# Optimization experiments

Hardware: AMD Instinct MI355X
Metric: run time of the kernel (lower is better)

## Reference

```python
import jax, jax.numpy as jnp
import numpy as np

S, B, D, H, L = 512, 64, 1024, 1024, 2
EPS = 1e-5  # torch LayerNorm default


def setup_inputs() -> dict:
    key = jax.random.key(0)
    ks = jax.random.split(key, 6)
    gain = (1.0 / H) ** 0.5  # matches LSTM._init uniform(-gain, gain)
    return {
        "inputs": jax.random.normal(ks[0], (S, B, D), jnp.float32),
        "h0": jax.random.normal(ks[1], (L, B, H), jnp.float32),
        "c0": jax.random.normal(ks[2], (L, B, H), jnp.float32),
        "wx": jax.random.uniform(ks[3], (L, D, 4 * H), jnp.float32, -gain, gain),
        "wh": jax.random.uniform(ks[4], (L, H, 4 * H), jnp.float32, -gain, gain),
        "bias": jax.random.uniform(ks[5], (L, 4 * H), jnp.float32, -gain, gain),
        "ln_gamma": jnp.ones((L, 4, H), jnp.float32),
        "ln_beta": jnp.zeros((L, 4, H), jnp.float32),
    }


def _run_layer(x, h, c, wx_l, wh_l, b_l, g_l, bb_l):
    # Precompute the input projection for all timesteps (same math as per-step matmul).
    xg = jnp.einsum('sbd,dk->sbk', x, wx_l) + b_l  # [S, B, 4H]

    def step(carry, xg_t):
        h, c = carry
        gate = xg_t + h @ wh_l                      # [B, 4H]
        gate = gate.reshape(-1, 4, H)               # [B, 4, H] per-gate
        mu = gate.mean(-1, keepdims=True)
        var = gate.var(-1, keepdims=True)           # biased, as torch LayerNorm
        gate = (gate - mu) * jax.lax.rsqrt(var + EPS) * g_l + bb_l
        i, f, o, u = gate[:, 0], gate[:, 1], gate[:, 2], gate[:, 3]
        c = jax.nn.sigmoid(f) * c + jax.nn.sigmoid(i) * jnp.tanh(u)
        h = jax.nn.sigmoid(o) * jnp.tanh(c)
        return (h, c), h

    (h, c), ys = jax.lax.scan(step, (h, c), xg)
    return ys, h, c


def reference(inputs, h0, c0, wx, wh, bias, ln_gamma, ln_beta):
    x = inputs
    hs, cs = [], []
    for l in range(L):  # small fixed layer loop (structurally distinct weights)
        x, h, c = _run_layer(x, h0[l], c0[l], wx[l], wh[l], bias[l],
                             ln_gamma[l], ln_beta[l])
        hs.append(h)
        cs.append(c)
    # matches (x, [stacked h, stacked c]) with list_next_state=False
    return x, jnp.stack(hs, 0), jnp.stack(cs, 0)
```

## Files before the change

kernel.cpp:

```cpp
#include <hip/hip_runtime.h>
#include <cstdint>
#include <cstddef>

#define SEQ 512
#define BAT 64
#define DIM 1024
#define HID 1024
#define NLAYER 2
#define NGATE 4096
#define EPS_LN 1e-5f
#define KSPLIT 12
#define PART_STRIDE (BAT * NGATE)
#define LO_SCALE 4096.0f
#define LO_INV (1.0f / 4096.0f)

typedef __attribute__((ext_vector_type(8))) _Float16 f16x8;
typedef __attribute__((ext_vector_type(4))) float f32x4;

__device__ __forceinline__ unsigned short f2h(float f) {
    _Float16 h = (_Float16)f;
    unsigned short u; __builtin_memcpy(&u, &h, 2); return u;
}
__device__ __forceinline__ float h2f(unsigned short u) {
    _Float16 h; __builtin_memcpy(&h, &u, 2); return (float)h;
}


__global__ void init_hc_kernel(const float* __restrict__ h0,
                               const float* __restrict__ c0,
                               float* __restrict__ hbuf,
                               float* __restrict__ cbuf) {
    int i = blockIdx.x * blockDim.x + threadIdx.x;
    hbuf[i] = h0[i];
    cbuf[i] = c0[i];
}

__global__ __launch_bounds__(256) void prepack_w_kernel(
    const float* __restrict__ wx, const float* __restrict__ wh,
    unsigned short* __restrict__ wp)
{
    int gid = blockIdx.x * 256 + threadIdx.x;
    int lane = gid & 63;
    int kc   = (gid >> 6) & 31;
    int nt   = (gid >> 11) & 255;
    int mat  = (gid >> 19) & 1;
    int l    = (gid >> 20) & 1;
    const float* src = (mat ? wh : wx) + (size_t)l * ((size_t)DIM * NGATE);
    int col = nt * 16 + (lane & 15);
    int kr0 = kc * 32 + 8 * (lane >> 4);
    unsigned hp[4], lp[4];
    #pragma unroll
    for (int i = 0; i < 4; i++) {
        float v0 = src[(size_t)(kr0 + 2 * i) * NGATE + col];
        float v1 = src[(size_t)(kr0 + 2 * i + 1) * NGATE + col];
        unsigned short h0 = f2h(v0), h1 = f2h(v1);
        unsigned short l0 = f2h(LO_SCALE * (v0 - h2f(h0)));
        unsigned short l1 = f2h(LO_SCALE * (v1 - h2f(h1)));
        hp[i] = (unsigned)h0 | ((unsigned)h1 << 16);
        lp[i] = (unsigned)l0 | ((unsigned)l1 << 16);
    }
    size_t inner = (((size_t)nt * 32 + kc) * 64 + lane) * 8;
    unsigned short* dh = wp + (((size_t)(l * 4 + mat * 2 + 0)) << 22) + inner;
    unsigned short* dl = wp + (((size_t)(l * 4 + mat * 2 + 1)) << 22) + inner;
    *(uint4*)dh = make_uint4(hp[0], hp[1], hp[2], hp[3]);
    *(uint4*)dl = make_uint4(lp[0], lp[1], lp[2], lp[3]);
}

template<bool DUAL>
__device__ __forceinline__ void gates_body(
    const float* __restrict__ A0, const float* __restrict__ A1,
    const unsigned short* __restrict__ wpl, float* __restrict__ part,
    unsigned short* a_hi, unsigned short* a_lo)
{
    const int ntb = blockIdx.x;
    const int kb  = blockIdx.y;
    int mat, k0, klen;
    if (DUAL) { mat = kb >> 2;       k0 = (kb & 3) * 256; klen = 256; }
    else      { mat = (kb >> 1) & 1; k0 = (kb & 1) * 512; klen = 512; }
    const float* __restrict__ Asrc = mat ? A1 : A0;
    const unsigned short* __restrict__ Wbase =
        wpl + (((size_t)(mat * 2 + (DUAL ? 0 : 1))) << 22);

    const int tid  = threadIdx.x;
    const int lane = tid & 63;
    const int w    = tid >> 6;
    const int m0w  = (w >> 1) * 32;
    const int nh   = w & 1;
    const int lrow = lane & 15;
    const int lg   = lane >> 4;

    f32x4 acc[2][4];
    f32x4 accl[2][4];
    #pragma unroll
    for (int mi = 0; mi < 2; mi++)
        #pragma unroll
        for (int ni = 0; ni < 4; ni++) {
            acc[mi][ni] = (f32x4){0.f, 0.f, 0.f, 0.f};
            accl[mi][ni] = (f32x4){0.f, 0.f, 0.f, 0.f};
        }

    const int sr = tid >> 2;
    const int sq = (tid & 3) * 32;

    for (int kc0 = 0; kc0 < klen; kc0 += 128) {
        __syncthreads();
        {
            const float* s = Asrc + (size_t)sr * 1024 + k0 + kc0 + sq;
            float4 q[8];
            #pragma unroll
            for (int i = 0; i < 8; i++) q[i] = *(const float4*)(s + 4 * i);
            unsigned hp[16], lp[16];
            #pragma unroll
            for (int i = 0; i < 8; i++) {
                unsigned short h0 = f2h(q[i].x), h1 = f2h(q[i].y);
                unsigned short h2 = f2h(q[i].z), h3 = f2h(q[i].w);
                hp[2 * i]     = (unsigned)h0 | ((unsigned)h1 << 16);
                hp[2 * i + 1] = (unsigned)h2 | ((unsigned)h3 << 16);
                if (DUAL) {
                    unsigned short l0 = f2h(LO_SCALE * (q[i].x - h2f(h0)));
                    unsigned short l1 = f2h(LO_SCALE * (q[i].y - h2f(h1)));
                    unsigned short l2 = f2h(LO_SCALE * (q[i].z - h2f(h2)));
                    unsigned short l3 = f2h(LO_SCALE * (q[i].w - h2f(h3)));
                    lp[2 * i]     = (unsigned)l0 | ((unsigned)l1 << 16);
                    lp[2 * i + 1] = (unsigned)l2 | ((unsigned)l3 << 16);
                }
            }
            unsigned base = sr * 256 + sq * 2;
            #pragma unroll
            for (int i = 0; i < 4; i++) {
                unsigned off = (base + 16 * i) ^ ((sr & 7) << 4);
                *(uint4*)((char*)a_hi + off) =
                    make_uint4(hp[4 * i], hp[4 * i + 1], hp[4 * i + 2], hp[4 * i + 3]);
                if (DUAL)
                    *(uint4*)((char*)a_lo + off) =
                        make_uint4(lp[4 * i], lp[4 * i + 1], lp[4 * i + 2], lp[4 * i + 3]);
            }
        }
        __syncthreads();

        const int kcgb = (k0 + kc0) >> 5;
        #pragma unroll
        for (int kk = 0; kk < 4; kk++) {
            f16x8 bfr[4];
            #pragma unroll
            for (int ni = 0; ni < 4; ni++) {
                int ntg = ntb * 8 + nh * 4 + ni;
                const unsigned short* wptr =
                    Wbase + ((((size_t)ntg * 32) + (size_t)(kcgb + kk)) * 64 + lane) * 8;
                bfr[ni] = *(const f16x8*)wptr;
            }
            f16x8 ah[2], al[2];
            #pragma unroll
            for (int mi = 0; mi < 2; mi++) {
                int row = m0w + mi * 16 + lrow;
                unsigned off = ((unsigned)(row * 256 + kk * 64 + lg * 16)) ^ ((row & 7) << 4);
                ah[mi] = *(const f16x8*)((const char*)a_hi + off);
                if (DUAL) al[mi] = *(const f16x8*)((const char*)a_lo + off);
            }
            #pragma unroll
            for (int mi = 0; mi < 2; mi++)
                #pragma unroll
                for (int ni = 0; ni < 4; ni++) {
                    acc[mi][ni] = __builtin_amdgcn_mfma_f32_16x16x32_f16(
                        ah[mi], bfr[ni], acc[mi][ni], 0, 0, 0);
                    if (DUAL)
                        accl[mi][ni] = __builtin_amdgcn_mfma_f32_16x16x32_f16(
                            al[mi], bfr[ni], accl[mi][ni], 0, 0, 0);
                }
        }
    }

    float* __restrict__ pp = part + (size_t)kb * PART_STRIDE;
    #pragma unroll
    for (int mi = 0; mi < 2; mi++)
        #pragma unroll
        for (int ni = 0; ni < 4; ni++) {
            int brow = m0w + mi * 16 + 4 * lg;
            int col  = ntb * 128 + nh * 64 + ni * 16 + lrow;
            #pragma unroll
            for (int r = 0; r < 4; r++) {
                float v = DUAL ? (acc[mi][ni][r] + accl[mi][ni][r] * LO_INV)
                               : (acc[mi][ni][r] * LO_INV);
                pp[(size_t)(brow + r) * NGATE + col] = v;
            }
        }
}

__global__ __launch_bounds__(256) void gates_mfma_kernel(
    const float* __restrict__ A0,
    const float* __restrict__ A1,
    const unsigned short* __restrict__ wpl,
    float* __restrict__ part)
{
    __shared__ __align__(16) unsigned short a_hi[64 * 128];
    __shared__ __align__(16) unsigned short a_lo[64 * 128];
    if (blockIdx.y < 8) gates_body<true>(A0, A1, wpl, part, a_hi, a_lo);
    else                gates_body<false>(A0, A1, wpl, part, a_hi, a_lo);
}

__global__ __launch_bounds__(1024) void update_kernel(
    const float* __restrict__ part,
    const float* __restrict__ bias,
    const float* __restrict__ gamma,
    const float* __restrict__ beta,
    float* __restrict__ cbuf,
    float* __restrict__ hbuf,
    float* __restrict__ y_out,
    float* __restrict__ hs_out,
    float* __restrict__ cs_out)
{
    int b = blockIdx.x;
    int j = threadIdx.x;
    float raw[4], s[4], q[4];
    #pragma unroll
    for (int g = 0; g < 4; g++) {
        int col = g * 1024 + j;
        float v = bias[col];
        #pragma unroll
        for (int p = 0; p < KSPLIT; p++)
            v += part[(size_t)p * PART_STRIDE + (size_t)b * 4096 + col];
        raw[g] = v; s[g] = v; q[g] = v * v;
    }
    #pragma unroll
    for (int off = 32; off > 0; off >>= 1) {
        #pragma unroll
        for (int g = 0; g < 4; g++) {
            s[g] += __shfl_down(s[g], off);
            q[g] += __shfl_down(q[g], off);
        }
    }
    __shared__ float red[16][8];
    __shared__ float stats[8];
    int wave = j >> 6, lane = j & 63;
    if (lane == 0) {
        #pragma unroll
        for (int g = 0; g < 4; g++) { red[wave][g] = s[g]; red[wave][4 + g] = q[g]; }
    }
    __syncthreads();
    if (j == 0) {
        float ts[8] = {0,0,0,0,0,0,0,0};
        for (int w = 0; w < 16; w++)
            for (int g = 0; g < 8; g++) ts[g] += red[w][g];
        #pragma unroll
        for (int g = 0; g < 4; g++) {
            float mu  = ts[g] * (1.0f / 1024.0f);
            float var = ts[4 + g] * (1.0f / 1024.0f) - mu * mu;
            stats[g] = mu;
            stats[4 + g] = rsqrtf(fmaxf(var, 0.0f) + EPS_LN);
        }
    }
    __syncthreads();
    float gh[4];
    #pragma unroll
    for (int g = 0; g < 4; g++) {
        int col = g * 1024 + j;
        gh[g] = (raw[g] - stats[g]) * stats[4 + g] * gamma[col] + beta[col];
    }
    float c_old = cbuf[b * 1024 + j];
    float ig = 1.f / (1.f + __expf(-gh[0]));
    float fg = 1.f / (1.f + __expf(-gh[1]));
    float og = 1.f / (1.f + __expf(-gh[2]));
    float c_new = fg * c_old + ig * tanhf(gh[3]);
    float h_new = og * tanhf(c_new);
    cbuf[b * 1024 + j] = c_new;
    hbuf[b * 1024 + j] = h_new;
    y_out[b * 1024 + j] = h_new;
    if (hs_out) { hs_out[b * 1024 + j] = h_new; cs_out[b * 1024 + j] = c_new; }
}


extern "C" void kernel_launch(void* const* d_in, const int* in_sizes, int n_in,
                              void* d_out, int out_size, void* d_ws, size_t ws_size,
                              hipStream_t stream) {
    const float* inputs = (const float*)d_in[0];
    const float* h0     = (const float*)d_in[1];
    const float* c0     = (const float*)d_in[2];
    const float* wx     = (const float*)d_in[3];
    const float* wh     = (const float*)d_in[4];
    const float* bias   = (const float*)d_in[5];
    const float* gamma  = (const float*)d_in[6];
    const float* beta   = (const float*)d_in[7];
    float* dout = (float*)d_out;

    unsigned short* wp = (unsigned short*)d_ws;
    float* part = (float*)(wp + ((size_t)8 << 22));
    float* hbuf = part + (size_t)KSPLIT * PART_STRIDE;
    float* cbuf = hbuf + NLAYER * BAT * HID;

    prepack_w_kernel<<<8192, 256, 0, stream>>>(wx, wh, wp);
    init_hc_kernel<<<512, 256, 0, stream>>>(h0, c0, hbuf, cbuf);

    const int BH = BAT * HID;
    const int XOUT = SEQ * BAT * HID;
    for (int t = 0; t < SEQ; t++) {
        for (int l = 0; l < NLAYER; l++) {
            const float* a0 = (l == 0) ? (inputs + (size_t)t * BH)
                                       : (dout + (size_t)t * BH);
            gates_mfma_kernel<<<dim3(32, KSPLIT), 256, 0, stream>>>(
                a0, hbuf + l * BH, wp + ((size_t)l << 24), part);
            update_kernel<<<64, 1024, 0, stream>>>(
                part,
                bias + l * 4096, gamma + l * 4096, beta + l * 4096,
                cbuf + l * BH, hbuf + l * BH,
                dout + (size_t)t * BH,
                (t == SEQ - 1) ? (dout + XOUT + l * BH) : nullptr,
                (t == SEQ - 1) ? (dout + XOUT + NLAYER * BH + l * BH) : nullptr);
        }
    }
}
```

Before: 25.20 ms.

## Stage whole K-slice of activations once, halve N tile, double-buffer weight loads

The gates kernel now converts and stores its entire K slice of activations (256 or 512 columns) to shared memory in a single pass, with one barrier instead of a barrier-separated loop of 128-column chunks. Each block now covers 64 gate columns instead of 128, so the grid doubles to 64x12 blocks, and launch bounds request 2 blocks per CU. Weight fragments are register double-buffered, with the next K group's load issued before the current MFMAs. The aim is more parallelism across the MI355X's CUs and less sync and load latency per step. The cost is each block redoing the activation fp16 conversion for half as many columns, plus a 64 KB shared buffer that may limit occupancy.

```diff
diff --git a/kernel.cpp b/kernel.cpp
--- a/kernel.cpp
+++ b/kernel.cpp
@@ -70,13 +70,15 @@
 __device__ __forceinline__ void gates_body(
     const float* __restrict__ A0, const float* __restrict__ A1,
     const unsigned short* __restrict__ wpl, float* __restrict__ part,
-    unsigned short* a_hi, unsigned short* a_lo)
+    unsigned short* __restrict__ abuf)
 {
+    constexpr int KLEN = DUAL ? 256 : 512;
+    constexpr int G = KLEN / 32;
     const int ntb = blockIdx.x;
     const int kb  = blockIdx.y;
-    int mat, k0, klen;
-    if (DUAL) { mat = kb >> 2;       k0 = (kb & 3) * 256; klen = 256; }
-    else      { mat = (kb >> 1) & 1; k0 = (kb & 1) * 512; klen = 512; }
+    int mat, k0;
+    if (DUAL) { mat = kb >> 2;       k0 = (kb & 3) * 256; }
+    else      { mat = (kb >> 1) & 1; k0 = (kb & 1) * 512; }
     const float* __restrict__ Asrc = mat ? A1 : A0;
     const unsigned short* __restrict__ Wbase =
         wpl + (((size_t)(mat * 2 + (DUAL ? 0 : 1))) << 22);
@@ -89,94 +91,99 @@
     const int lrow = lane & 15;
     const int lg   = lane >> 4;
 
-    f32x4 acc[2][4];
-    f32x4 accl[2][4];
+    unsigned short* __restrict__ alo = abuf + 64 * 256;
+
+    {
+        const int sr = tid >> 2;
+        const int sq = (tid & 3) * (KLEN / 4);
+        const float* s = Asrc + (size_t)sr * 1024 + k0 + sq;
+        const unsigned rowb = (unsigned)sr * (KLEN * 2);
+        const unsigned sw = (unsigned)((sr & 7) << 4);
+        #pragma unroll
+        for (int j = 0; j < KLEN / 32; j++) {
+            float4 a = *(const float4*)(s + 8 * j);
+            float4 b = *(const float4*)(s + 8 * j + 4);
+            unsigned short h[8];
+            h[0] = f2h(a.x); h[1] = f2h(a.y); h[2] = f2h(a.z); h[3] = f2h(a.w);
+            h[4] = f2h(b.x); h[5] = f2h(b.y); h[6] = f2h(b.z); h[7] = f2h(b.w);
+            uint4 hv = make_uint4((unsigned)h[0] | ((unsigned)h[1] << 16),
+                                  (unsigned)h[2] | ((unsigned)h[3] << 16),
+                                  (unsigned)h[4] | ((unsigned)h[5] << 16),
+                                  (unsigned)h[6] | ((unsigned)h[7] << 16));
+            unsigned off = (rowb + (unsigned)(sq + 8 * j) * 2) ^ sw;
+            *(uint4*)((char*)abuf + off) = hv;
+            if (DUAL) {
+                unsigned short l[8];
+                l[0] = f2h(LO_SCALE * (a.x - h2f(h[0])));
+                l[1] = f2h(LO_SCALE * (a.y - h2f(h[1])));
+                l[2] = f2h(LO_SCALE * (a.z - h2f(h[2])));
+                l[3] = f2h(LO_SCALE * (a.w - h2f(h[3])));
+                l[4] = f2h(LO_SCALE * (b.x - h2f(h[4])));
+                l[5] = f2h(LO_SCALE * (b.y - h2f(h[5])));
+                l[6] = f2h(LO_SCALE * (b.z - h2f(h[6])));
+                l[7] = f2h(LO_SCALE * (b.w - h2f(h[7])));
+                uint4 lv = make_uint4((unsigned)l[0] | ((unsigned)l[1] << 16),
+                                      (unsigned)l[2] | ((unsigned)l[3] << 16),
+                                      (unsigned)l[4] | ((unsigned)l[5] << 16),
+                                      (unsigned)l[6] | ((unsigned)l[7] << 16));
+                *(uint4*)((char*)alo + off) = lv;
+            }
+        }
+    }
+    __syncthreads();
+
+    const size_t kcg0 = (size_t)(k0 >> 5);
+    const int ntgb = ntb * 4 + nh * 2;
+    f32x4 acc[2][2], accl[2][2];
     #pragma unroll
     for (int mi = 0; mi < 2; mi++)
         #pragma unroll
-        for (int ni = 0; ni < 4; ni++) {
-            acc[mi][ni] = (f32x4){0.f, 0.f, 0.f, 0.f};
+        for (int ni = 0; ni < 2; ni++) {
+            acc[mi][ni]  = (f32x4){0.f, 0.f, 0.f, 0.f};
             accl[mi][ni] = (f32x4){0.f, 0.f, 0.f, 0.f};
         }
 
-    const int sr = tid >> 2;
-    const int sq = (tid & 3) * 32;
-
-    for (int kc0 = 0; kc0 < klen; kc0 += 128) {
-        __syncthreads();
-        {
-            const float* s = Asrc + (size_t)sr * 1024 + k0 + kc0 + sq;
-            float4 q[8];
+    f16x8 wv[2][2];
+    auto wload = [&](int g, int buf) {
+        #pragma unroll
+        for (int ni = 0; ni < 2; ni++)
+            wv[buf][ni] = *(const f16x8*)(Wbase +
+                (((size_t)(ntgb + ni) * 32 + kcg0 + (size_t)g) * 64 + lane) * 8);
+    };
+    wload(0, 0);
+
+    #pragma unroll
+    for (int g = 0; g < G; g++) {
+        if (g + 1 < G) wload(g + 1, (g + 1) & 1);
+        f16x8 ah[2], al[2];
+        #pragma unroll
+        for (int mi = 0; mi < 2; mi++) {
+            int row = m0w + mi * 16 + lrow;
+            unsigned off = (unsigned)row * (KLEN * 2) +
+                           (((unsigned)(g * 64 + lg * 16)) ^ ((unsigned)(row & 7) << 4));
+            ah[mi] = *(const f16x8*)((const char*)abuf + off);
+            if (DUAL) al[mi] = *(const f16x8*)((const char*)alo + off);
+        }
+        const int b = g & 1;
+        #pragma unroll
+        for (int mi = 0; mi < 2; mi++)
             #pragma unroll
-            for (int i = 0; i < 8; i++) q[i] = *(const float4*)(s + 4 * i);
-            unsigned hp[16], lp[16];
-            #pragma unroll
-            for (int i = 0; i < 8; i++) {
-                unsigned short h0 = f2h(q[i].x), h1 = f2h(q[i].y);
-                unsigned short h2 = f2h(q[i].z), h3 = f2h(q[i].w);
-                hp[2 * i]     = (unsigned)h0 | ((unsigned)h1 << 16);
-                hp[2 * i + 1] = (unsigned)h2 | ((unsigned)h3 << 16);
-                if (DUAL) {
-                    unsigned short l0 = f2h(LO_SCALE * (q[i].x - h2f(h0)));
-                    unsigned short l1 = f2h(LO_SCALE * (q[i].y - h2f(h1)));
-                    unsigned short l2 = f2h(LO_SCALE * (q[i].z - h2f(h2)));
-                    unsigned short l3 = f2h(LO_SCALE * (q[i].w - h2f(h3)));
-                    lp[2 * i]     = (unsigned)l0 | ((unsigned)l1 << 16);
-                    lp[2 * i + 1] = (unsigned)l2 | ((unsigned)l3 << 16);
-                }
+            for (int ni = 0; ni < 2; ni++) {
+                acc[mi][ni] = __builtin_amdgcn_mfma_f32_16x16x32_f16(
+                    ah[mi], wv[b][ni], acc[mi][ni], 0, 0, 0);
+                if (DUAL)
+                    accl[mi][ni] = __builtin_amdgcn_mfma_f32_16x16x32_f16(
+                        al[mi], wv[b][ni], accl[mi][ni], 0, 0, 0);
             }
-            unsigned base = sr * 256 + sq * 2;
-            #pragma unroll
-            for (int i = 0; i < 4; i++) {
-                unsigned off = (base + 16 * i) ^ ((sr & 7) << 4);
-                *(uint4*)((char*)a_hi + off) =
-                    make_uint4(hp[4 * i], hp[4 * i + 1], hp[4 * i + 2], hp[4 * i + 3]);
-                if (DUAL)
-                    *(uint4*)((char*)a_lo + off) =
-                        make_uint4(lp[4 * i], lp[4 * i + 1], lp[4 * i + 2], lp[4 * i + 3]);
-            }
-        }
-        __syncthreads();
-
-        const int kcgb = (k0 + kc0) >> 5;
-        #pragma unroll
-        for (int kk = 0; kk < 4; kk++) {
-            f16x8 bfr[4];
-            #pragma unroll
-            for (int ni = 0; ni < 4; ni++) {
-                int ntg = ntb * 8 + nh * 4 + ni;
-                const unsigned short* wptr =
-                    Wbase + ((((size_t)ntg * 32) + (size_t)(kcgb + kk)) * 64 + lane) * 8;
-                bfr[ni] = *(const f16x8*)wptr;
-            }
-            f16x8 ah[2], al[2];
-            #pragma unroll
-            for (int mi = 0; mi < 2; mi++) {
-                int row = m0w + mi * 16 + lrow;
-                unsigned off = ((unsigned)(row * 256 + kk * 64 + lg * 16)) ^ ((row & 7) << 4);
-                ah[mi] = *(const f16x8*)((const char*)a_hi + off);
-                if (DUAL) al[mi] = *(const f16x8*)((const char*)a_lo + off);
-            }
-            #pragma unroll
-            for (int mi = 0; mi < 2; mi++)
-                #pragma unroll
-                for (int ni = 0; ni < 4; ni++) {
-                    acc[mi][ni] = __builtin_amdgcn_mfma_f32_16x16x32_f16(
-                        ah[mi], bfr[ni], acc[mi][ni], 0, 0, 0);
-                    if (DUAL)
-                        accl[mi][ni] = __builtin_amdgcn_mfma_f32_16x16x32_f16(
-                            al[mi], bfr[ni], accl[mi][ni], 0, 0, 0);
-                }
-        }
     }
 
     float* __restrict__ pp = part + (size_t)kb * PART_STRIDE;
     #pragma unroll
     for (int mi = 0; mi < 2; mi++)
         #pragma unroll
-        for (int ni = 0; ni < 4; ni++) {
+        for (int ni = 0; ni < 2; ni++) {
             int brow = m0w + mi * 16 + 4 * lg;
-            int col  = ntb * 128 + nh * 64 + ni * 16 + lrow;
+            int col  = ntb * 64 + nh * 32 + ni * 16 + lrow;
             #pragma unroll
             for (int r = 0; r < 4; r++) {
                 float v = DUAL ? (acc[mi][ni][r] + accl[mi][ni][r] * LO_INV)
@@ -186,16 +193,15 @@
         }
 }
 
-__global__ __launch_bounds__(256) void gates_mfma_kernel(
+__global__ __launch_bounds__(256, 2) void gates_mfma_kernel(
     const float* __restrict__ A0,
     const float* __restrict__ A1,
     const unsigned short* __restrict__ wpl,
     float* __restrict__ part)
 {
-    __shared__ __align__(16) unsigned short a_hi[64 * 128];
-    __shared__ __align__(16) unsigned short a_lo[64 * 128];
-    if (blockIdx.y < 8) gates_body<true>(A0, A1, wpl, part, a_hi, a_lo);
-    else                gates_body<false>(A0, A1, wpl, part, a_hi, a_lo);
+    __shared__ __align__(16) unsigned short abuf[64 * 512];
+    if (blockIdx.y < 8) gates_body<true>(A0, A1, wpl, part, abuf);
+    else                gates_body<false>(A0, A1, wpl, part, abuf);
 }
 
 __global__ __launch_bounds__(1024) void update_kernel(
@@ -296,7 +302,7 @@
         for (int l = 0; l < NLAYER; l++) {
             const float* a0 = (l == 0) ? (inputs + (size_t)t * BH)
                                        : (dout + (size_t)t * BH);
-            gates_mfma_kernel<<<dim3(32, KSPLIT), 256, 0, stream>>>(
+            gates_mfma_kernel<<<dim3(64, KSPLIT), 256, 0, stream>>>(
                 a0, hbuf + l * BH, wp + ((size_t)l << 24), part);
             update_kernel<<<64, 1024, 0, stream>>>(
                 part,
```

Measured after the change: 29.36 ms. +16.5%, slower.
